# Optimization experiments

Hardware: AMD Instinct MI355X
Metric: run time of the kernel (lower is better)

## Reference

```python
import jax, jax.numpy as jnp
import numpy as np
from jax import lax

N, C_IN, H, W = 32, 128, 64, 64
C_OUT, KH, KW = 256, 3, 3
C_DIM = 64


def setup_inputs() -> dict:
    key = jax.random.key(0)
    k1, k2, k3, k4, k5 = jax.random.split(key, 5)
    return {
        "x": jax.random.normal(k1, (N, C_IN, H, W), dtype=jnp.float32),
        "c": jax.random.normal(k2, (N, C_DIM), dtype=jnp.float32),
        "weight": jax.random.normal(k3, (C_OUT, C_IN, KH, KW), dtype=jnp.float32),
        "c_weight": jax.random.normal(k4, (C_OUT, C_DIM), dtype=jnp.float32),
        "bias": jax.random.normal(k5, (C_OUT,), dtype=jnp.float32),
    }


def reference(x, c, weight, c_weight, bias):
    # Equivalent to the module's unfold + matmul path (groups=1, dilation=1,
    # zero padding=1, stride=1): a direct conv fused with the spatially
    # invariant context bias c @ c_weight^T and the channel bias.
    out = lax.conv_general_dilated(
        x, weight,
        window_strides=(1, 1),
        padding=((1, 1), (1, 1)),
        dimension_numbers=("NCHW", "OIHW", "NCHW"),
    )  # (N, C_out, H, W)
    ctx = jnp.einsum("nd,od->no", c, c_weight)  # (N, C_out), same at every spatial loc
    return out + ctx[:, :, None, None] + bias[None, :, None, None]
```

## Files before the change

kernel.cpp:

```cpp
#include <hip/hip_runtime.h>
#include <hip/hip_bf16.h>


#define NN   32
#define CIN  128
#define HH   64
#define WW   64
#define COUT 256
#define CDIM 64
#define HP   66
#define WP   66

#define XP_BYTES  ((size_t)NN*HP*WP*CIN*2)
#define WT_BYTES  ((size_t)9*COUT*CIN*2)
#define CTX_BYTES ((size_t)NN*COUT*4)
#define WS_NEEDED (XP_BYTES + WT_BYTES + CTX_BYTES)

typedef __attribute__((ext_vector_type(8))) short short8;
typedef __attribute__((ext_vector_type(4))) float float4v;

__device__ __forceinline__ void async16(const void* g, void* l) {
    __builtin_amdgcn_global_load_lds(
        (const __attribute__((address_space(1))) unsigned int*)g,
        (__attribute__((address_space(3))) unsigned int*)l, 16, 0, 0);
}

__global__ __launch_bounds__(256) void prep_all(
    const float* __restrict__ x, const float* __restrict__ c,
    const float* __restrict__ wgt, const float* __restrict__ cw,
    const float* __restrict__ bias,
    __hip_bfloat16* __restrict__ xP, __hip_bfloat16* __restrict__ wT,
    float* __restrict__ ctx)
{
    __shared__ float tile[CIN][65];
    int bid = blockIdx.x;
    int t   = threadIdx.x;

    if (bid < 2048) {
        int n = bid >> 6;
        int h = bid & 63;
        const float* xb = x + (size_t)n * CIN * HH * WW + (size_t)h * WW;

        int lane16 = t & 15, rgrp = t >> 4;
        #pragma unroll
        for (int i = 0; i < 8; ++i) {
            int ci = rgrp + i * 16;
            float4v v = *(const float4v*)(xb + (size_t)ci * (HH * WW) + lane16 * 4);
            int w0 = lane16 * 4;
            tile[ci][w0]     = v.x;
            tile[ci][w0 + 1] = v.y;
            tile[ci][w0 + 2] = v.z;
            tile[ci][w0 + 3] = v.w;
        }
        __syncthreads();

        int oct = t & 3, w = t >> 2;
        __hip_bfloat16* db = xP + (((size_t)n * HP + (h + 1)) * WP + (w + 1)) * CIN;
        #pragma unroll
        for (int p = 0; p < 4; ++p) {
            int ci0 = p * 32 + oct * 8;
            union { short8 v; __hip_bfloat16 b[8]; } u;
            #pragma unroll
            for (int j = 0; j < 8; ++j)
                u.b[j] = __float2bfloat16(tile[ci0 + j][w]);
            *(short8*)(db + ci0) = u.v;
        }
    } else if (bid < 2568) {
        int g = (bid - 2048) * 256 + t;
        int n   = g / 4160;
        int rem = g - n * 4160;
        int pi  = rem >> 4;
        int oct = rem & 15;
        int hh, ww;
        if (pi < 132) { hh = (pi >= 66) ? 65 : 0; ww = pi % 66; }
        else { int p2 = pi - 132; ww = (p2 >= 64) ? 65 : 0; hh = 1 + (p2 & 63); }
        short8 z = {};
        *(short8*)(xP + (((size_t)n * HP + hh) * WP + ww) * CIN + oct * 8) = z;
    } else {
        int b2 = bid - 2568;
        if (b2 < 1152) {
            int idx = b2 * 256 + t;
            int ci  = idx & 127;
            int co  = (idx >> 7) & 255;
            int tap = idx >> 15;
            wT[idx] = __float2bfloat16(wgt[((size_t)co * CIN + ci) * 9 + tap]);
        } else {
            int idx = (b2 - 1152) * 256 + t;
            int co = idx & 255, n = idx >> 8;
            float a = bias[co];
            #pragma unroll 8
            for (int d = 0; d < CDIM; ++d) a += c[n * CDIM + d] * cw[co * CDIM + d];
            ctx[idx] = a;
        }
    }
}

__global__ __launch_bounds__(512) void conv_mfma(
    const __hip_bfloat16* __restrict__ xP,
    const __hip_bfloat16* __restrict__ wT,
    const float* __restrict__ ctx,
    float* __restrict__ out)
{
    __shared__ __align__(16) short A_s[2][16384];
    __shared__ __align__(16) short B_s[2][16384];

    int bid = blockIdx.x;
    int mt  = (bid & 7) * 64 + (bid >> 3);
    int n   = mt >> 4;
    int h0  = (mt & 15) << 2;

    int tid  = threadIdx.x;
    int lane = tid & 63, wv = tid >> 6;
    int wm = (wv & 1) * 128;
    int wn = (wv >> 1) * 64;

    int rr  = tid >> 3;
    int q8  = ((tid & 7) ^ (rr & 7)) << 3;
    int stg = tid * 8;
    const __hip_bfloat16* xA = xP + ((size_t)(n * HP + h0) * WP + rr) * CIN + q8;
    const __hip_bfloat16* xB = wT + (size_t)rr * CIN + q8;

    int l15   = lane & 15;
    int rowA  = (wm + l15) << 6;
    int rowB  = (wn + l15) << 6;
    int cofs0 = (((lane >> 4)    ) ^ (lane & 7)) << 3;
    int cofs1 = (((lane >> 4) + 4) ^ (lane & 7)) << 3;

    float4v acc[8][4] = {};

    #pragma unroll
    for (int i = 0; i < 4; ++i) {
        async16(xA + i * (WP * CIN), &A_s[0][i * 4096 + stg]);
        async16(xB + i * (64 * CIN), &B_s[0][i * 4096 + stg]);
    }

    for (int s = 0; s < 18; ++s) {
        int cur = s & 1;
        __syncthreads();

        if (s < 17) {
            int s1  = s + 1;
            int tap = s1 >> 1, kb = s1 & 1;
            int kh  = (tap * 11) >> 5;
            int kw  = tap - kh * 3;
            const __hip_bfloat16* a1 = xA + (kh * WP + kw) * CIN + kb * 64;
            const __hip_bfloat16* b1 = xB + tap * (COUT * CIN) + kb * 64;
            short* Ad = A_s[cur ^ 1];
            short* Bd = B_s[cur ^ 1];
            #pragma unroll
            for (int i = 0; i < 4; ++i) {
                async16(a1 + i * (WP * CIN), Ad + i * 4096 + stg);
                async16(b1 + i * (64 * CIN), Bd + i * 4096 + stg);
            }
        }

        const short* Ab = A_s[cur];
        const short* Bb = B_s[cur];
        #pragma unroll
        for (int kk = 0; kk < 2; ++kk) {
            int cofs = kk ? cofs1 : cofs0;
            short8 aF[8], bF[4];
            #pragma unroll
            for (int mi = 0; mi < 8; ++mi)
                aF[mi] = *(const short8*)&Ab[rowA + mi * 1024 + cofs];
            #pragma unroll
            for (int ni = 0; ni < 4; ++ni)
                bF[ni] = *(const short8*)&Bb[rowB + ni * 1024 + cofs];
            #pragma unroll
            for (int mi = 0; mi < 8; ++mi)
                #pragma unroll
                for (int ni = 0; ni < 4; ++ni)
                    acc[mi][ni] = __builtin_amdgcn_mfma_f32_16x16x32_bf16(
                        aF[mi], bF[ni], acc[mi][ni], 0, 0, 0);
        }
    }

    #pragma unroll
    for (int ni = 0; ni < 4; ++ni) {
        int co = wn + ni * 16 + l15;
        float cv = ctx[n * COUT + co];
        float* ob = out + ((size_t)n * COUT + co) * (HH * WW);
        #pragma unroll
        for (int mi = 0; mi < 8; ++mi) {
            int rp = wm + mi * 16 + ((lane >> 4) << 2);
            int hh = h0 + (rp >> 6);
            int ww = rp & 63;
            float4v v = acc[mi][ni] + cv;
            *(float4v*)&ob[hh * WW + ww] = v;
        }
    }
}

__global__ __launch_bounds__(256) void contextual_conv_f32(
    const float* __restrict__ x, const float* __restrict__ c,
    const float* __restrict__ wgt, const float* __restrict__ cw,
    const float* __restrict__ bias, float* __restrict__ out)
{
    int idx = blockIdx.x * 256 + threadIdx.x;
    int w = idx & 63, h = (idx >> 6) & 63, cb = (idx >> 12) & 63, n = idx >> 18;
    float acc[4];
    #pragma unroll
    for (int j = 0; j < 4; ++j) acc[j] = bias[cb + j * 64];
    const float* cp = c + n * CDIM;
    for (int d = 0; d < CDIM; ++d) {
        float cv = cp[d];
        #pragma unroll
        for (int j = 0; j < 4; ++j) acc[j] += cv * cw[(cb + j * 64) * CDIM + d];
    }
    const float* xn = x + (size_t)n * (CIN * HH * WW);
    for (int ci = 0; ci < CIN; ++ci) {
        const float* xc = xn + ci * (HH * WW);
        float wv[4][9];
        #pragma unroll
        for (int j = 0; j < 4; ++j) {
            const float* wp = wgt + ((cb + j * 64) * CIN + ci) * 9;
            #pragma unroll
            for (int k = 0; k < 9; ++k) wv[j][k] = wp[k];
        }
        #pragma unroll
        for (int kh = 0; kh < 3; ++kh) {
            int hh = h + kh - 1;
            if (hh < 0 || hh >= HH) continue;
            const float* xr = xc + hh * WW;
            #pragma unroll
            for (int kw = 0; kw < 3; ++kw) {
                int ww = w + kw - 1;
                if (ww < 0 || ww >= WW) continue;
                float xv = xr[ww];
                #pragma unroll
                for (int j = 0; j < 4; ++j) acc[j] += xv * wv[j][kh * 3 + kw];
            }
        }
    }
    size_t obase = (size_t)n * (COUT * HH * WW) + (size_t)h * WW + w;
    #pragma unroll
    for (int j = 0; j < 4; ++j)
        out[obase + (size_t)(cb + j * 64) * (HH * WW)] = acc[j];
}

extern "C" void kernel_launch(void* const* d_in, const int* in_sizes, int n_in,
                              void* d_out, int out_size, void* d_ws, size_t ws_size,
                              hipStream_t stream) {
    const float* x    = (const float*)d_in[0];
    const float* c    = (const float*)d_in[1];
    const float* wgt  = (const float*)d_in[2];
    const float* cw   = (const float*)d_in[3];
    const float* bias = (const float*)d_in[4];
    float* out = (float*)d_out;

    if (ws_size < WS_NEEDED) {
        const int total_threads = NN * 64 * HH * WW;
        contextual_conv_f32<<<total_threads / 256, 256, 0, stream>>>(x, c, wgt, cw, bias, out);
        return;
    }

    char* ws = (char*)d_ws;
    __hip_bfloat16* xP = (__hip_bfloat16*)ws;
    __hip_bfloat16* wT = (__hip_bfloat16*)(ws + XP_BYTES);
    float*          cx = (float*)(ws + XP_BYTES + WT_BYTES);

    prep_all <<<3752, 256, 0, stream>>>(x, c, wgt, cw, bias, xP, wT, cx);
    conv_mfma<<<512, 512, 0, stream>>>(xP, wT, cx, out);
}
```

Measured before the change: 268.2 us.

## Restructure conv GEMM main loop into four-phase ping-pong with staggered prefetch

Replaces the simple double-buffered K loop with a four-quadrant schedule. Each 64-wide K step is split into four MFMA sub-blocks. LDS fragment loads and async global-to-LDS copies are interleaved between them, fenced by raw s_barrier, and s_setprio raises wave priority around the MFMA bursts. The B operand is now prefetched two steps ahead and reuses the current buffer, while A is prefetched one step ahead. The intent is to overlap memory traffic with matrix math and drop the single syncthreads stall, at the cost of more barriers and fragile hand-coded vmcnt accounting.

Measured after the change: 267.4 us. Within noise of the previous version (-0.3%).

```diff
diff --git a/kernel.cpp b/kernel.cpp
--- a/kernel.cpp
+++ b/kernel.cpp
@@ -24,6 +24,9 @@
         (const __attribute__((address_space(1))) unsigned int*)g,
         (__attribute__((address_space(3))) unsigned int*)l, 16, 0, 0);
 }
+
+#define BAR()      __builtin_amdgcn_s_barrier()
+#define SETPRIO(x) __builtin_amdgcn_s_setprio(x)
 
 __global__ __launch_bounds__(256) void prep_all(
     const float* __restrict__ x, const float* __restrict__ c,
@@ -129,50 +132,126 @@
     float4v acc[8][4] = {};
 
     #pragma unroll
-    for (int i = 0; i < 4; ++i) {
+    for (int i = 0; i < 4; ++i)
+        async16(xB + i * (64 * CIN), &B_s[0][i * 4096 + stg]);
+    #pragma unroll
+    for (int i = 0; i < 4; ++i)
         async16(xA + i * (WP * CIN), &A_s[0][i * 4096 + stg]);
-        async16(xB + i * (64 * CIN), &B_s[0][i * 4096 + stg]);
-    }
-
-    for (int s = 0; s < 18; ++s) {
-        int cur = s & 1;
-        __syncthreads();
-
-        if (s < 17) {
-            int s1  = s + 1;
-            int tap = s1 >> 1, kb = s1 & 1;
-            int kh  = (tap * 11) >> 5;
-            int kw  = tap - kh * 3;
-            const __hip_bfloat16* a1 = xA + (kh * WP + kw) * CIN + kb * 64;
-            const __hip_bfloat16* b1 = xB + tap * (COUT * CIN) + kb * 64;
-            short* Ad = A_s[cur ^ 1];
-            short* Bd = B_s[cur ^ 1];
-            #pragma unroll
-            for (int i = 0; i < 4; ++i) {
-                async16(a1 + i * (WP * CIN), Ad + i * 4096 + stg);
-                async16(b1 + i * (64 * CIN), Bd + i * 4096 + stg);
-            }
-        }
-
-        const short* Ab = A_s[cur];
-        const short* Bb = B_s[cur];
-        #pragma unroll
-        for (int kk = 0; kk < 2; ++kk) {
-            int cofs = kk ? cofs1 : cofs0;
-            short8 aF[8], bF[4];
-            #pragma unroll
-            for (int mi = 0; mi < 8; ++mi)
-                aF[mi] = *(const short8*)&Ab[rowA + mi * 1024 + cofs];
-            #pragma unroll
-            for (int ni = 0; ni < 4; ++ni)
-                bF[ni] = *(const short8*)&Bb[rowB + ni * 1024 + cofs];
-            #pragma unroll
-            for (int mi = 0; mi < 8; ++mi)
-                #pragma unroll
-                for (int ni = 0; ni < 4; ++ni)
-                    acc[mi][ni] = __builtin_amdgcn_mfma_f32_16x16x32_bf16(
-                        aF[mi], bF[ni], acc[mi][ni], 0, 0, 0);
-        }
+    #pragma unroll
+    for (int i = 0; i < 4; ++i)
+        async16(xB + 64 + i * (64 * CIN), &B_s[1][i * 4096 + stg]);
+    asm volatile("s_waitcnt vmcnt(4)" ::: "memory");
+    BAR();
+
+    #pragma unroll 2
+    for (int kt = 0; kt < 18; ++kt) {
+        int cur = kt & 1;
+        const short* Ac = A_s[cur];
+        const short* Bc = B_s[cur];
+
+        int ktA = kt + 1, tapA = ktA >> 1, kbA = ktA & 1;
+        int khA = (tapA * 11) >> 5, kwA = tapA - khA * 3;
+        const __hip_bfloat16* aS = xA + (khA * WP + kwA) * CIN + kbA * 64;
+        short* Ad = A_s[cur ^ 1];
+        int ktB = kt + 2, tapB = ktB >> 1, kbB = ktB & 1;
+        const __hip_bfloat16* bS = xB + (size_t)tapB * (COUT * CIN) + kbB * 64;
+        short* Bd = B_s[cur];
+
+        short8 a0[4][2], a1[4][2], b0[2][2], b1[2][2];
+
+        #pragma unroll
+        for (int mi = 0; mi < 4; ++mi) {
+            a0[mi][0] = *(const short8*)&Ac[rowA + mi * 1024 + cofs0];
+            a0[mi][1] = *(const short8*)&Ac[rowA + mi * 1024 + cofs1];
+        }
+        #pragma unroll
+        for (int ni = 0; ni < 2; ++ni) {
+            b0[ni][0] = *(const short8*)&Bc[rowB + ni * 1024 + cofs0];
+            b0[ni][1] = *(const short8*)&Bc[rowB + ni * 1024 + cofs1];
+        }
+        if (ktA < 18) {
+            async16(aS,                &Ad[0 * 4096 + stg]);
+            async16(aS + 1 * (WP * CIN), &Ad[1 * 4096 + stg]);
+        }
+        BAR();
+        SETPRIO(1);
+        #pragma unroll
+        for (int mi = 0; mi < 4; ++mi)
+            #pragma unroll
+            for (int ni = 0; ni < 2; ++ni) {
+                acc[mi][ni] = __builtin_amdgcn_mfma_f32_16x16x32_bf16(
+                    a0[mi][0], b0[ni][0], acc[mi][ni], 0, 0, 0);
+                acc[mi][ni] = __builtin_amdgcn_mfma_f32_16x16x32_bf16(
+                    a0[mi][1], b0[ni][1], acc[mi][ni], 0, 0, 0);
+            }
+        SETPRIO(0);
+        BAR();
+
+        #pragma unroll
+        for (int ni = 0; ni < 2; ++ni) {
+            b1[ni][0] = *(const short8*)&Bc[rowB + (ni + 2) * 1024 + cofs0];
+            b1[ni][1] = *(const short8*)&Bc[rowB + (ni + 2) * 1024 + cofs1];
+        }
+        if (ktA < 18) {
+            async16(aS + 2 * (WP * CIN), &Ad[2 * 4096 + stg]);
+            async16(aS + 3 * (WP * CIN), &Ad[3 * 4096 + stg]);
+        }
+        BAR();
+        SETPRIO(1);
+        #pragma unroll
+        for (int mi = 0; mi < 4; ++mi)
+            #pragma unroll
+            for (int ni = 0; ni < 2; ++ni) {
+                acc[mi][ni + 2] = __builtin_amdgcn_mfma_f32_16x16x32_bf16(
+                    a0[mi][0], b1[ni][0], acc[mi][ni + 2], 0, 0, 0);
+                acc[mi][ni + 2] = __builtin_amdgcn_mfma_f32_16x16x32_bf16(
+                    a0[mi][1], b1[ni][1], acc[mi][ni + 2], 0, 0, 0);
+            }
+        SETPRIO(0);
+        BAR();
+
+        #pragma unroll
+        for (int mi = 0; mi < 4; ++mi) {
+            a1[mi][0] = *(const short8*)&Ac[rowA + (mi + 4) * 1024 + cofs0];
+            a1[mi][1] = *(const short8*)&Ac[rowA + (mi + 4) * 1024 + cofs1];
+        }
+        if (ktB < 18) {
+            async16(bS,                  &Bd[0 * 4096 + stg]);
+            async16(bS + 1 * (64 * CIN), &Bd[1 * 4096 + stg]);
+        }
+        BAR();
+        SETPRIO(1);
+        #pragma unroll
+        for (int mi = 0; mi < 4; ++mi)
+            #pragma unroll
+            for (int ni = 0; ni < 2; ++ni) {
+                acc[mi + 4][ni] = __builtin_amdgcn_mfma_f32_16x16x32_bf16(
+                    a1[mi][0], b0[ni][0], acc[mi + 4][ni], 0, 0, 0);
+                acc[mi + 4][ni] = __builtin_amdgcn_mfma_f32_16x16x32_bf16(
+                    a1[mi][1], b0[ni][1], acc[mi + 4][ni], 0, 0, 0);
+            }
+        SETPRIO(0);
+        BAR();
+
+        if (ktB < 18) {
+            async16(bS + 2 * (64 * CIN), &Bd[2 * 4096 + stg]);
+            async16(bS + 3 * (64 * CIN), &Bd[3 * 4096 + stg]);
+        }
+        if (kt <= 15) asm volatile("s_waitcnt vmcnt(4)" ::: "memory");
+        else          asm volatile("s_waitcnt vmcnt(0)" ::: "memory");
+        BAR();
+        SETPRIO(1);
+        #pragma unroll
+        for (int mi = 0; mi < 4; ++mi)
+            #pragma unroll
+            for (int ni = 0; ni < 2; ++ni) {
+                acc[mi + 4][ni + 2] = __builtin_amdgcn_mfma_f32_16x16x32_bf16(
+                    a1[mi][0], b1[ni][0], acc[mi + 4][ni + 2], 0, 0, 0);
+                acc[mi + 4][ni + 2] = __builtin_amdgcn_mfma_f32_16x16x32_bf16(
+                    a1[mi][1], b1[ni][1], acc[mi + 4][ni + 2], 0, 0, 0);
+            }
+        SETPRIO(0);
+        BAR();
     }
 
     #pragma unroll
```

## Stage full padded input halo in LDS once and triple-buffer weight slices

Applied to the files above, without the earlier changes.

The conv kernel now loads the entire 6x66x128 padded input halo for a 4-row output tile into LDS once, and reads the shifted windows for all nine taps from it. Before, it re-fetched an A tile from global memory for every tap and K half. Weights are streamed in smaller 32-wide K slices through a 3-deep ring with a prefetch distance of two, using a single raw barrier per step and s_waitcnt instead of __syncthreads. MFMA sections are wrapped in s_setprio. This cuts global and L2 traffic for the input, but LDS use grows to about 150KB, which limits occupancy to one block per CU. There are also more K steps with less MFMA work between barriers.

After: 270.3 us. Within noise of the previous version (+0.8%).

```diff
diff --git a/kernel.cpp b/kernel.cpp
--- a/kernel.cpp
+++ b/kernel.cpp
@@ -24,6 +24,9 @@
         (const __attribute__((address_space(1))) unsigned int*)g,
         (__attribute__((address_space(3))) unsigned int*)l, 16, 0, 0);
 }
+
+#define BAR()      __builtin_amdgcn_s_barrier()
+#define SETPRIO(x) __builtin_amdgcn_s_setprio(x)
 
 __global__ __launch_bounds__(256) void prep_all(
     const float* __restrict__ x, const float* __restrict__ c,
@@ -101,8 +104,8 @@
     const float* __restrict__ ctx,
     float* __restrict__ out)
 {
-    __shared__ __align__(16) short A_s[2][16384];
-    __shared__ __align__(16) short B_s[2][16384];
+    __shared__ __align__(16) short A_s[50688];
+    __shared__ __align__(16) short B_s[3][8192];
 
     int bid = blockIdx.x;
     int mt  = (bid & 7) * 64 + (bid >> 3);
@@ -113,66 +116,81 @@
     int lane = tid & 63, wv = tid >> 6;
     int wm = (wv & 1) * 128;
     int wn = (wv >> 1) * 64;
-
-    int rr  = tid >> 3;
-    int q8  = ((tid & 7) ^ (rr & 7)) << 3;
-    int stg = tid * 8;
-    const __hip_bfloat16* xA = xP + ((size_t)(n * HP + h0) * WP + rr) * CIN + q8;
-    const __hip_bfloat16* xB = wT + (size_t)rr * CIN + q8;
-
-    int l15   = lane & 15;
-    int rowA  = (wm + l15) << 6;
-    int rowB  = (wn + l15) << 6;
-    int cofs0 = (((lane >> 4)    ) ^ (lane & 7)) << 3;
-    int cofs1 = (((lane >> 4) + 4) ^ (lane & 7)) << 3;
+    int l15 = lane & 15, lu = lane >> 4;
+
+    const __hip_bfloat16* xPn = xP + (size_t)(n * HP + h0) * WP * CIN;
+    #pragma unroll
+    for (int rnd = 0; rnd < 13; ++rnd) {
+        int g = rnd * 512 + tid;
+        if (g < 6336) {
+            int r  = g >> 4, cc = g & 15;
+            int hh = r / 66;
+            int ww = r - hh * 66;
+            int so = ((cc & 7) ^ (r & 7)) | (cc & 8);
+            async16(xPn + ((size_t)hh * WP + ww) * CIN + so * 8, &A_s[g * 8]);
+        }
+    }
+
+    int coS = tid >> 2, clS = tid & 3;
+    int soS = clS ^ ((coS >> 1) & 3);
+    const __hip_bfloat16* bsrc0 = wT + (size_t)coS * CIN + soS * 8;
+
+    #pragma unroll
+    for (int b = 0; b < 2; ++b) {
+        const __hip_bfloat16* bs = bsrc0 + b * 32;
+        async16(bs,             &B_s[b][tid * 8]);
+        async16(bs + 128 * CIN, &B_s[b][(512 + tid) * 8]);
+    }
+    asm volatile("s_waitcnt vmcnt(2)" ::: "memory");
+
+    int ohc = wm >> 6;
+    int pbB = lu ^ ((l15 >> 1) & 3);
 
     float4v acc[8][4] = {};
 
-    #pragma unroll
-    for (int i = 0; i < 4; ++i) {
-        async16(xA + i * (WP * CIN), &A_s[0][i * 4096 + stg]);
-        async16(xB + i * (64 * CIN), &B_s[0][i * 4096 + stg]);
-    }
-
-    for (int s = 0; s < 18; ++s) {
-        int cur = s & 1;
-        __syncthreads();
-
-        if (s < 17) {
-            int s1  = s + 1;
-            int tap = s1 >> 1, kb = s1 & 1;
-            int kh  = (tap * 11) >> 5;
-            int kw  = tap - kh * 3;
-            const __hip_bfloat16* a1 = xA + (kh * WP + kw) * CIN + kb * 64;
-            const __hip_bfloat16* b1 = xB + tap * (COUT * CIN) + kb * 64;
-            short* Ad = A_s[cur ^ 1];
-            short* Bd = B_s[cur ^ 1];
-            #pragma unroll
-            for (int i = 0; i < 4; ++i) {
-                async16(a1 + i * (WP * CIN), Ad + i * 4096 + stg);
-                async16(b1 + i * (64 * CIN), Bd + i * 4096 + stg);
-            }
-        }
-
-        const short* Ab = A_s[cur];
-        const short* Bb = B_s[cur];
-        #pragma unroll
-        for (int kk = 0; kk < 2; ++kk) {
-            int cofs = kk ? cofs1 : cofs0;
-            short8 aF[8], bF[4];
-            #pragma unroll
-            for (int mi = 0; mi < 8; ++mi)
-                aF[mi] = *(const short8*)&Ab[rowA + mi * 1024 + cofs];
+    #pragma unroll 3
+    for (int kt = 0; kt < 36; ++kt) {
+        BAR();
+
+        if (kt < 34) {
+            int t2 = kt + 2, tap2 = t2 >> 2, kb2 = t2 & 3;
+            const __hip_bfloat16* bs = bsrc0 + (size_t)tap2 * (COUT * CIN) + kb2 * 32;
+            short* Bd = &B_s[(kt + 2) % 3][0];
+            async16(bs,             Bd + tid * 8);
+            async16(bs + 128 * CIN, Bd + (512 + tid) * 8);
+        }
+
+        int tap = kt >> 2, kb = kt & 3;
+        int kh  = (tap * 11) >> 5, kw = tap - kh * 3;
+        int rb0 = (ohc + kh) * 66 + l15 + kw;
+        int cL  = kb * 4 + lu;
+        int c7  = cL & 7, cg = cL & 8;
+        const short* Bb = &B_s[kt % 3][0];
+
+        short8 aF[8], bF[4];
+        #pragma unroll
+        for (int mi = 0; mi < 8; ++mi) {
+            int r    = rb0 + (mi >> 2) * 66 + (mi & 3) * 16;
+            int phys = (c7 ^ (r & 7)) | cg;
+            aF[mi] = *(const short8*)&A_s[r * 128 + phys * 8];
+        }
+        #pragma unroll
+        for (int ni = 0; ni < 4; ++ni) {
+            int co = wn + ni * 16 + l15;
+            bF[ni] = *(const short8*)&Bb[co * 32 + pbB * 8];
+        }
+
+        SETPRIO(1);
+        #pragma unroll
+        for (int mi = 0; mi < 8; ++mi)
             #pragma unroll
             for (int ni = 0; ni < 4; ++ni)
-                bF[ni] = *(const short8*)&Bb[rowB + ni * 1024 + cofs];
-            #pragma unroll
-            for (int mi = 0; mi < 8; ++mi)
-                #pragma unroll
-                for (int ni = 0; ni < 4; ++ni)
-                    acc[mi][ni] = __builtin_amdgcn_mfma_f32_16x16x32_bf16(
-                        aF[mi], bF[ni], acc[mi][ni], 0, 0, 0);
-        }
+                acc[mi][ni] = __builtin_amdgcn_mfma_f32_16x16x32_bf16(
+                    aF[mi], bF[ni], acc[mi][ni], 0, 0, 0);
+        SETPRIO(0);
+
+        if (kt < 34) asm volatile("s_waitcnt vmcnt(2)" ::: "memory");
+        else         asm volatile("s_waitcnt vmcnt(0)" ::: "memory");
     }
 
     #pragma unroll
@@ -182,7 +200,7 @@
         float* ob = out + ((size_t)n * COUT + co) * (HH * WW);
         #pragma unroll
         for (int mi = 0; mi < 8; ++mi) {
-            int rp = wm + mi * 16 + ((lane >> 4) << 2);
+            int rp = wm + mi * 16 + (lu << 2);
             int hh = h0 + (rp >> 6);
             int ww = rp & 63;
             float4v v = acc[mi][ni] + cv;
```
